# Performance work log

Hardware: AMD Instinct MI355X
Metric: run time of the kernel (lower is better)

## Reference

```python
import jax, jax.numpy as jnp
import numpy as np

LN_EPS = 1e-5


def _ln(x, g, b):
    m = x.mean(-1, keepdims=True)
    v = ((x - m) ** 2).mean(-1, keepdims=True)
    return (x - m) * jax.lax.rsqrt(v + LN_EPS) * g + b


def setup_inputs() -> dict:
    key = jax.random.key(0)
    ks = jax.random.split(key, 8)
    B, S, T, Ds, Dt, H = 2, 1024, 1024, 128, 64, 64

    def w(k, shp):
        return jax.random.normal(k, shp, dtype=jnp.float32) * 0.05

    return {
        "source_features": jax.random.normal(ks[0], (B, S, Ds), dtype=jnp.float32),
        "target_features": jax.random.normal(ks[1], (B, T, Dt), dtype=jnp.float32),
        # source_adapter: Linear(Ds,H) -> LN(H) -> ReLU -> Linear(H,H)
        "sW1": w(ks[2], (Ds, H)), "sb1": jnp.zeros(H), "sg": jnp.ones(H), "sbeta": jnp.zeros(H),
        "sW2": w(ks[3], (H, H)), "sb2": jnp.zeros(H),
        # target_adapter: Linear(Dt,H) -> LN(H) -> ReLU -> Linear(H,H)
        "tW1": w(ks[4], (Dt, H)), "tb1": jnp.zeros(H), "tg": jnp.ones(H), "tbeta": jnp.zeros(H),
        "tW2": w(ks[5], (H, H)), "tb2": jnp.zeros(H),
        # city_features: Linear(2H,H) -> LN(H) -> ReLU
        "cW": w(ks[6], (2 * H, H)), "cb": jnp.zeros(H), "cg": jnp.ones(H), "cbeta": jnp.zeros(H),
        # similarity_module: Linear(H,1) -> Sigmoid
        "simW": w(ks[7], (H, 1)), "simb": jnp.zeros(1),
    }


def reference(source_features, target_features,
              sW1, sb1, sg, sbeta, sW2, sb2,
              tW1, tb1, tg, tbeta, tW2, tb2,
              cW, cb, cg, cbeta, simW, simb):
    H = sW2.shape[1]
    s_ad = jax.nn.relu(_ln(source_features @ sW1 + sb1, sg, sbeta)) @ sW2 + sb2  # [B,S,H]
    t_ad = jax.nn.relu(_ln(target_features @ tW1 + tb1, tg, tbeta)) @ tW2 + tb2  # [B,T,H]

    # concat order in torch is [target, source] on the last dim; split the
    # Linear(2H,H) weight so the [B,T,S,2H] concat is never materialized.
    cW_t, cW_s = cW[:H], cW[H:]
    pre = (t_ad @ cW_t)[:, :, None, :] + (s_ad @ cW_s)[:, None, :, :] + cb  # [B,T,S,H]
    h = jax.nn.relu(_ln(pre, cg, cbeta))
    scores = jax.nn.sigmoid((h @ simW)[..., 0] + simb[0])  # [B,T,S]

    attn = jax.nn.softmax(scores, axis=-1)
    transferred = jnp.einsum('bts,bsh->bth', attn, s_ad)
    gate = jax.nn.sigmoid(t_ad.mean(-1, keepdims=True))
    adapted = t_ad * (1.0 - gate) + transferred * gate  # hidden_dim == target_dim: no proj
    return adapted, scores
```

## Files before the change

### kernel.cpp

```cpp
#include <hip/hip_runtime.h>
#include <math.h>

#define BN 2
#define SN 1024
#define TN 1024
#define DS 128
#define DT 64
#define HN 64
#define LN_EPS 1e-5f

typedef float v2f __attribute__((ext_vector_type(2)));

__device__ __forceinline__ float wave_sum(float v) {
#pragma unroll
  for (int m = 32; m >= 1; m >>= 1) v += __shfl_xor(v, m, 64);
  return v;
}

__device__ __forceinline__ v2f lo2(float4 v) { v2f r = {v.x, v.y}; return r; }
__device__ __forceinline__ v2f hi2(float4 v) { v2f r = {v.z, v.w}; return r; }

__global__ __launch_bounds__(256) void k_adapters(
    const float* __restrict__ src, const float* __restrict__ tgt,
    const float* __restrict__ sW1, const float* __restrict__ sb1,
    const float* __restrict__ sg, const float* __restrict__ sbeta,
    const float* __restrict__ sW2, const float* __restrict__ sb2,
    const float* __restrict__ tW1, const float* __restrict__ tb1,
    const float* __restrict__ tg, const float* __restrict__ tbeta,
    const float* __restrict__ tW2, const float* __restrict__ tb2,
    const float* __restrict__ cW, const float* __restrict__ cb,
    float* __restrict__ s_ad, float* __restrict__ sc, float* __restrict__ sstats,
    float* __restrict__ t_ad, float* __restrict__ tc, float* __restrict__ tstats)
{
  __shared__ float xbuf[4][DS];
  __shared__ float rbuf[4][HN];
  int w = threadIdx.x >> 6, lane = threadIdx.x & 63;

  if (blockIdx.x < 512) {
    int row = blockIdx.x * 4 + w;
    xbuf[w][lane]      = src[row * DS + lane];
    xbuf[w][lane + 64] = src[row * DS + 64 + lane];
    float a0 = 0.f, a1 = 0.f, a2_ = 0.f, a3 = 0.f;
#pragma unroll 8
    for (int k = 0; k < DS; k += 4) {
      a0  = fmaf(xbuf[w][k + 0], sW1[(k + 0) * HN + lane], a0);
      a1  = fmaf(xbuf[w][k + 1], sW1[(k + 1) * HN + lane], a1);
      a2_ = fmaf(xbuf[w][k + 2], sW1[(k + 2) * HN + lane], a2_);
      a3  = fmaf(xbuf[w][k + 3], sW1[(k + 3) * HN + lane], a3);
    }
    float h1 = ((a0 + a1) + (a2_ + a3)) + sb1[lane];
    float s1 = wave_sum(h1), s2 = wave_sum(h1 * h1);
    float m = s1 * (1.f / HN);
    float var = s2 * (1.f / HN) - m * m;
    float r = fmaxf(0.f, (h1 - m) * rsqrtf(var + LN_EPS) * sg[lane] + sbeta[lane]);
    rbuf[w][lane] = r;
    float b0 = 0.f, b1 = 0.f, b2 = 0.f, b3 = 0.f;
#pragma unroll 4
    for (int j = 0; j < HN; j += 4) {
      b0 = fmaf(rbuf[w][j + 0], sW2[(j + 0) * HN + lane], b0);
      b1 = fmaf(rbuf[w][j + 1], sW2[(j + 1) * HN + lane], b1);
      b2 = fmaf(rbuf[w][j + 2], sW2[(j + 2) * HN + lane], b2);
      b3 = fmaf(rbuf[w][j + 3], sW2[(j + 3) * HN + lane], b3);
    }
    float a2 = ((b0 + b1) + (b2 + b3)) + sb2[lane];
    s_ad[row * HN + lane] = a2;
    rbuf[w][lane] = a2;
    float c0 = 0.f, c1 = 0.f, c2 = 0.f, c3 = 0.f;
#pragma unroll 4
    for (int j = 0; j < HN; j += 4) {
      c0 = fmaf(rbuf[w][j + 0], cW[(HN + j + 0) * HN + lane], c0);
      c1 = fmaf(rbuf[w][j + 1], cW[(HN + j + 1) * HN + lane], c1);
      c2 = fmaf(rbuf[w][j + 2], cW[(HN + j + 2) * HN + lane], c2);
      c3 = fmaf(rbuf[w][j + 3], cW[(HN + j + 3) * HN + lane], c3);
    }
    float scv = (c0 + c1) + (c2 + c3);
    sc[row * HN + lane] = scv;
    float bs = wave_sum(scv), qs = wave_sum(scv * scv);
    if (lane == 0) { sstats[row * 2] = bs; sstats[row * 2 + 1] = qs; }
  } else {
    int row = (blockIdx.x - 512) * 4 + w;
    xbuf[w][lane] = tgt[row * DT + lane];
    float a0 = 0.f, a1 = 0.f, a2_ = 0.f, a3 = 0.f;
#pragma unroll 4
    for (int k = 0; k < DT; k += 4) {
      a0  = fmaf(xbuf[w][k + 0], tW1[(k + 0) * HN + lane], a0);
      a1  = fmaf(xbuf[w][k + 1], tW1[(k + 1) * HN + lane], a1);
      a2_ = fmaf(xbuf[w][k + 2], tW1[(k + 2) * HN + lane], a2_);
      a3  = fmaf(xbuf[w][k + 3], tW1[(k + 3) * HN + lane], a3);
    }
    float h1 = ((a0 + a1) + (a2_ + a3)) + tb1[lane];
    float s1 = wave_sum(h1), s2 = wave_sum(h1 * h1);
    float m = s1 * (1.f / HN);
    float var = s2 * (1.f / HN) - m * m;
    float r = fmaxf(0.f, (h1 - m) * rsqrtf(var + LN_EPS) * tg[lane] + tbeta[lane]);
    rbuf[w][lane] = r;
    float b0 = 0.f, b1 = 0.f, b2 = 0.f, b3 = 0.f;
#pragma unroll 4
    for (int j = 0; j < HN; j += 4) {
      b0 = fmaf(rbuf[w][j + 0], tW2[(j + 0) * HN + lane], b0);
      b1 = fmaf(rbuf[w][j + 1], tW2[(j + 1) * HN + lane], b1);
      b2 = fmaf(rbuf[w][j + 2], tW2[(j + 2) * HN + lane], b2);
      b3 = fmaf(rbuf[w][j + 3], tW2[(j + 3) * HN + lane], b3);
    }
    float a2 = ((b0 + b1) + (b2 + b3)) + tb2[lane];
    t_ad[row * HN + lane] = a2;
    float asum = wave_sum(a2);
    float gate = 1.f / (1.f + __expf(-asum * (1.f / HN)));
    rbuf[w][lane] = a2;
    float c0 = 0.f, c1 = 0.f, c2 = 0.f, c3 = 0.f;
#pragma unroll 4
    for (int j = 0; j < HN; j += 4) {
      c0 = fmaf(rbuf[w][j + 0], cW[(j + 0) * HN + lane], c0);
      c1 = fmaf(rbuf[w][j + 1], cW[(j + 1) * HN + lane], c1);
      c2 = fmaf(rbuf[w][j + 2], cW[(j + 2) * HN + lane], c2);
      c3 = fmaf(rbuf[w][j + 3], cW[(j + 3) * HN + lane], c3);
    }
    float tcv = ((c0 + c1) + (c2 + c3)) + cb[lane];
    tc[row * HN + lane] = tcv;
    float A = wave_sum(tcv), Q = wave_sum(tcv * tcv);
    if (lane == 0) { tstats[row * 3] = A; tstats[row * 3 + 1] = Q; tstats[row * 3 + 2] = gate; }
  }
}

#define ROWDW 68
__global__ __launch_bounds__(512) void k_scores(
    const float* __restrict__ cg, const float* __restrict__ cbeta,
    const float* __restrict__ simW, const float* __restrict__ simb,
    const float* __restrict__ sc, const float* __restrict__ sstats,
    const float* __restrict__ tc, const float* __restrict__ tstats,
    float* __restrict__ out_scores)
{
  __shared__ float tile[64 * ROWDW];
  int tid = threadIdx.x;
  int w = tid >> 6, lane = tid & 63;
  int sblk = blockIdx.x & 15;
  int tblk = (blockIdx.x >> 4) & 63;
  int b    = blockIdx.x >> 10;
  int t0 = tblk * 16 + w * 2;
  int rt0 = __builtin_amdgcn_readfirstlane(b * TN + t0);
  int rt1 = rt0 + 1;
  int s0 = sblk * 64;

  float A0  = tstats[rt0 * 3 + 0];
  float Qt0 = tstats[rt0 * 3 + 1];
  float A1  = tstats[rt1 * 3 + 0];
  float Qt1 = tstats[rt1 * 3 + 1];
  const float4* tq0 = (const float4*)(tc + rt0 * HN);
  const float4* tq1 = (const float4*)(tc + rt1 * HN);
  const float4* cgq = (const float4*)cg;
  const float4* cbq = (const float4*)cbeta;
  const float4* swq = (const float4*)simW;
  float simb0 = simb[0];

  const float4* scg = (const float4*)(sc + b * SN * HN);

  {
    int r0s = tid >> 4, gs = tid & 15;
    float4 v0 = scg[(s0 + r0s) * 16 + gs];
    float4 v1 = scg[(s0 + r0s + 32) * 16 + gs];
    *(float4*)&tile[r0s * ROWDW + gs * 4] = v0;
    *(float4*)&tile[(r0s + 32) * ROWDW + gs * 4] = v1;
  }
  __syncthreads();

  const v2f zero2 = {0.f, 0.f};
  const float* tb_ = &tile[lane * ROWDW];
  int s = s0 + lane;
  float2 bq = *(const float2*)&sstats[(b * SN + s) * 2];

  v2f D0a = zero2, D0b = zero2, D1a = zero2, D1b = zero2;
#pragma unroll
  for (int g = 0; g < 16; ++g) {
    float4 v = *(const float4*)&tb_[g * 4];
    float4 ta = tq0[g]; float4 tbv = tq1[g];
    D0a = __builtin_elementwise_fma(lo2(ta),  lo2(v), D0a);
    D0b = __builtin_elementwise_fma(hi2(ta),  hi2(v), D0b);
    D1a = __builtin_elementwise_fma(lo2(tbv), lo2(v), D1a);
    D1b = __builtin_elementwise_fma(hi2(tbv), hi2(v), D1b);
  }
  v2f Ds0 = D0a + D0b, Ds1 = D1a + D1b;
  float D_0 = Ds0.x + Ds0.y;
  float D_1 = Ds1.x + Ds1.y;

  float mean0  = (A0 + bq.x) * (1.f / HN);
  float var0   = (Qt0 + bq.y + 2.f * D_0) * (1.f / HN) - mean0 * mean0;
  float alpha0 = rsqrtf(var0 + LN_EPS);
  float mean1  = (A1 + bq.x) * (1.f / HN);
  float var1   = (Qt1 + bq.y + 2.f * D_1) * (1.f / HN) - mean1 * mean1;
  float alpha1 = rsqrtf(var1 + LN_EPS);

  v2f m0 = {mean0, mean0}, a0v = {alpha0, alpha0};
  v2f m1 = {mean1, mean1}, a1v = {alpha1, alpha1};
  v2f dt0a = zero2, dt0b = zero2, dt1a = zero2, dt1b = zero2;

#pragma unroll
  for (int g = 0; g < 16; ++g) {
    float4 v  = *(const float4*)&tb_[g * 4];
    float4 c4 = cgq[g]; float4 b4 = cbq[g]; float4 w4 = swq[g];
    float4 ta = tq0[g]; float4 tbv = tq1[g];
    { v2f u = lo2(v) + lo2(ta);  v2f z = u - m0; v2f P = a0v * lo2(c4);
      v2f n = __builtin_elementwise_fma(z, P, lo2(b4));
      v2f r = __builtin_elementwise_max(n, zero2);
      dt0a = __builtin_elementwise_fma(r, lo2(w4), dt0a); }
    { v2f u = hi2(v) + hi2(ta);  v2f z = u - m0; v2f P = a0v * hi2(c4);
      v2f n = __builtin_elementwise_fma(z, P, hi2(b4));
      v2f r = __builtin_elementwise_max(n, zero2);
      dt0b = __builtin_elementwise_fma(r, hi2(w4), dt0b); }
    { v2f u = lo2(v) + lo2(tbv); v2f z = u - m1; v2f P = a1v * lo2(c4);
      v2f n = __builtin_elementwise_fma(z, P, lo2(b4));
      v2f r = __builtin_elementwise_max(n, zero2);
      dt1a = __builtin_elementwise_fma(r, lo2(w4), dt1a); }
    { v2f u = hi2(v) + hi2(tbv); v2f z = u - m1; v2f P = a1v * hi2(c4);
      v2f n = __builtin_elementwise_fma(z, P, hi2(b4));
      v2f r = __builtin_elementwise_max(n, zero2);
      dt1b = __builtin_elementwise_fma(r, hi2(w4), dt1b); }
  }
  v2f dd0 = dt0a + dt0b, dd1 = dt1a + dt1b;
  float dot0 = dd0.x + dd0.y;
  float dot1 = dd1.x + dd1.y;
  float score0 = 1.f / (1.f + __expf(-(dot0 + simb0)));
  float score1 = 1.f / (1.f + __expf(-(dot1 + simb0)));
  out_scores[rt0 * SN + s] = score0;
  out_scores[rt1 * SN + s] = score1;
}

__global__ __launch_bounds__(256, 4) void k_xfer(
    const float* __restrict__ scores, const float* __restrict__ s_ad,
    float* __restrict__ xpart, float* __restrict__ epart)
{
  __shared__ float eLDS[4][16][64];
  __shared__ float part[4][16][64];
  __shared__ float esum[4][16];
  int tid = threadIdx.x;
  int w = __builtin_amdgcn_readfirstlane(tid >> 6);
  int lane = tid & 63;
  int sblk = blockIdx.x & 3;
  int tblk = (blockIdx.x >> 2) & 63;
  int b    = blockIdx.x >> 8;
  int t0 = tblk * 16;
  int soff = sblk * 256 + w * 64;

#pragma unroll 4
  for (int t = 0; t < 16; ++t) {
    int rt = __builtin_amdgcn_readfirstlane(b * TN + t0 + t);
    float ev = __expf(scores[rt * SN + soff + lane]);
    eLDS[w][t][lane] = ev;
    float es = wave_sum(ev);
    if (lane == 0) esum[w][t] = es;
  }

  const float* sadb = s_ad + b * SN * HN;
  float acc[16];
#pragma unroll
  for (int t = 0; t < 16; ++t) acc[t] = 0.f;
#pragma unroll 4
  for (int si4 = 0; si4 < 16; ++si4) {
    int sbase = soff + si4 * 4;
    float sv0 = sadb[(sbase + 0) * HN + lane];
    float sv1 = sadb[(sbase + 1) * HN + lane];
    float sv2 = sadb[(sbase + 2) * HN + lane];
    float sv3 = sadb[(sbase + 3) * HN + lane];
#pragma unroll
    for (int t = 0; t < 16; ++t) {
      float4 e4 = *(const float4*)&eLDS[w][t][si4 * 4];
      acc[t] = fmaf(e4.x, sv0, acc[t]);
      acc[t] = fmaf(e4.y, sv1, acc[t]);
      acc[t] = fmaf(e4.z, sv2, acc[t]);
      acc[t] = fmaf(e4.w, sv3, acc[t]);
    }
  }

#pragma unroll
  for (int t = 0; t < 16; ++t) part[w][t][lane] = acc[t];
  __syncthreads();
#pragma unroll
  for (int k = 0; k < 4; ++k) {
    int c2 = tid + k * 256;
    int t = c2 >> 6, h = c2 & 63;
    float sum = part[0][t][h] + part[1][t][h] + part[2][t][h] + part[3][t][h];
    int rt = b * TN + t0 + t;
    xpart[(rt * 4 + sblk) * HN + h] = sum;
  }
  if (tid < 16) {
    float es = esum[0][tid] + esum[1][tid] + esum[2][tid] + esum[3][tid];
    int rt = b * TN + t0 + tid;
    epart[rt * 4 + sblk] = es;
  }
}

__global__ __launch_bounds__(256) void k_final(
    const float* __restrict__ xpart, const float* __restrict__ epart,
    const float* __restrict__ t_ad, const float* __restrict__ tstats,
    float* __restrict__ out_adapted)
{
  int tid = threadIdx.x;
  int tl = tid >> 6, h = tid & 63;
  int rt = blockIdx.x * 4 + tl;
  float x = xpart[(rt * 4 + 0) * HN + h] + xpart[(rt * 4 + 1) * HN + h]
          + xpart[(rt * 4 + 2) * HN + h] + xpart[(rt * 4 + 3) * HN + h];
  float es = epart[rt * 4 + 0] + epart[rt * 4 + 1]
           + epart[rt * 4 + 2] + epart[rt * 4 + 3];
  float tr = x / es;
  float gate = tstats[rt * 3 + 2];
  float tad = t_ad[rt * HN + h];
  out_adapted[rt * HN + h] = tad * (1.f - gate) + tr * gate;
}

extern "C" void kernel_launch(void* const* d_in, const int* in_sizes, int n_in,
                              void* d_out, int out_size, void* d_ws, size_t ws_size,
                              hipStream_t stream) {
  const float* src   = (const float*)d_in[0];
  const float* tgt   = (const float*)d_in[1];
  const float* sW1   = (const float*)d_in[2];
  const float* sb1   = (const float*)d_in[3];
  const float* sg    = (const float*)d_in[4];
  const float* sbeta = (const float*)d_in[5];
  const float* sW2   = (const float*)d_in[6];
  const float* sb2   = (const float*)d_in[7];
  const float* tW1   = (const float*)d_in[8];
  const float* tb1   = (const float*)d_in[9];
  const float* tg    = (const float*)d_in[10];
  const float* tbeta = (const float*)d_in[11];
  const float* tW2   = (const float*)d_in[12];
  const float* tb2   = (const float*)d_in[13];
  const float* cW    = (const float*)d_in[14];
  const float* cb    = (const float*)d_in[15];
  const float* cg    = (const float*)d_in[16];
  const float* cbeta = (const float*)d_in[17];
  const float* simW  = (const float*)d_in[18];
  const float* simb  = (const float*)d_in[19];

  float* ws     = (float*)d_ws;
  float* s_ad   = ws;
  float* sc     = ws + 131072;
  float* sstats = ws + 262144;
  float* t_ad   = ws + 266240;
  float* tc     = ws + 397312;
  float* tstats = ws + 528384;
  float* xpart  = ws + 534528;
  float* epart  = ws + 1058816;

  float* out_adapted = (float*)d_out;
  float* out_scores  = (float*)d_out + 131072;

  hipLaunchKernelGGL(k_adapters, dim3(1024), dim3(256), 0, stream,
                     src, tgt, sW1, sb1, sg, sbeta, sW2, sb2,
                     tW1, tb1, tg, tbeta, tW2, tb2, cW, cb,
                     s_ad, sc, sstats, t_ad, tc, tstats);
  hipLaunchKernelGGL(k_scores, dim3(BN * 64 * 16), dim3(512), 0, stream,
                     cg, cbeta, simW, simb, sc, sstats, tc, tstats, out_scores);
  hipLaunchKernelGGL(k_xfer, dim3(BN * 64 * 4), dim3(256), 0, stream,
                     out_scores, s_ad, xpart, epart);
  hipLaunchKernelGGL(k_final, dim3(512), dim3(256), 0, stream,
                     xpart, epart, t_ad, tstats, out_adapted);
}
```

Baseline: 154.3 us.

## Fuse softmax-transfer and final gating into one kernel using readlane broadcasts

Merges the transfer and final kernels into a single kernel in which each block handles 4 target rows across the full source range, with each wave covering a quarter of the sources. Exp scores are broadcast through readlane instead of being staged in LDS. This removes the xpart/epart workspace round trip and one kernel launch. In exchange each block reuses each s_ad load for only 4 target rows instead of 16, which raises L2 traffic for s_ad, and the per-iteration readlanes add scalar work.

```diff
diff --git a/kernel.cpp b/kernel.cpp
--- a/kernel.cpp
+++ b/kernel.cpp
@@ -19,6 +19,10 @@
 
 __device__ __forceinline__ v2f lo2(float4 v) { v2f r = {v.x, v.y}; return r; }
 __device__ __forceinline__ v2f hi2(float4 v) { v2f r = {v.z, v.w}; return r; }
+
+__device__ __forceinline__ float rl(float v, int l) {
+  return __int_as_float(__builtin_amdgcn_readlane(__float_as_int(v), l));
+}
 
 __global__ __launch_bounds__(256) void k_adapters(
     const float* __restrict__ src, const float* __restrict__ tgt,
@@ -224,82 +228,59 @@
   out_scores[rt1 * SN + s] = score1;
 }
 
-__global__ __launch_bounds__(256, 4) void k_xfer(
+__global__ __launch_bounds__(256) void k_transfer(
     const float* __restrict__ scores, const float* __restrict__ s_ad,
-    float* __restrict__ xpart, float* __restrict__ epart)
-{
-  __shared__ float eLDS[4][16][64];
-  __shared__ float part[4][16][64];
-  __shared__ float esum[4][16];
-  int tid = threadIdx.x;
-  int w = __builtin_amdgcn_readfirstlane(tid >> 6);
-  int lane = tid & 63;
-  int sblk = blockIdx.x & 3;
-  int tblk = (blockIdx.x >> 2) & 63;
-  int b    = blockIdx.x >> 8;
-  int t0 = tblk * 16;
-  int soff = sblk * 256 + w * 64;
-
-#pragma unroll 4
-  for (int t = 0; t < 16; ++t) {
-    int rt = __builtin_amdgcn_readfirstlane(b * TN + t0 + t);
-    float ev = __expf(scores[rt * SN + soff + lane]);
-    eLDS[w][t][lane] = ev;
-    float es = wave_sum(ev);
-    if (lane == 0) esum[w][t] = es;
-  }
-
-  const float* sadb = s_ad + b * SN * HN;
-  float acc[16];
-#pragma unroll
-  for (int t = 0; t < 16; ++t) acc[t] = 0.f;
-#pragma unroll 4
-  for (int si4 = 0; si4 < 16; ++si4) {
-    int sbase = soff + si4 * 4;
-    float sv0 = sadb[(sbase + 0) * HN + lane];
-    float sv1 = sadb[(sbase + 1) * HN + lane];
-    float sv2 = sadb[(sbase + 2) * HN + lane];
-    float sv3 = sadb[(sbase + 3) * HN + lane];
-#pragma unroll
-    for (int t = 0; t < 16; ++t) {
-      float4 e4 = *(const float4*)&eLDS[w][t][si4 * 4];
-      acc[t] = fmaf(e4.x, sv0, acc[t]);
-      acc[t] = fmaf(e4.y, sv1, acc[t]);
-      acc[t] = fmaf(e4.z, sv2, acc[t]);
-      acc[t] = fmaf(e4.w, sv3, acc[t]);
-    }
-  }
-
-#pragma unroll
-  for (int t = 0; t < 16; ++t) part[w][t][lane] = acc[t];
-  __syncthreads();
-#pragma unroll
-  for (int k = 0; k < 4; ++k) {
-    int c2 = tid + k * 256;
-    int t = c2 >> 6, h = c2 & 63;
-    float sum = part[0][t][h] + part[1][t][h] + part[2][t][h] + part[3][t][h];
-    int rt = b * TN + t0 + t;
-    xpart[(rt * 4 + sblk) * HN + h] = sum;
-  }
-  if (tid < 16) {
-    float es = esum[0][tid] + esum[1][tid] + esum[2][tid] + esum[3][tid];
-    int rt = b * TN + t0 + tid;
-    epart[rt * 4 + sblk] = es;
-  }
-}
-
-__global__ __launch_bounds__(256) void k_final(
-    const float* __restrict__ xpart, const float* __restrict__ epart,
     const float* __restrict__ t_ad, const float* __restrict__ tstats,
     float* __restrict__ out_adapted)
 {
+  __shared__ float part[4][4][64];
+  __shared__ float esumLDS[4][4];
   int tid = threadIdx.x;
-  int tl = tid >> 6, h = tid & 63;
-  int rt = blockIdx.x * 4 + tl;
-  float x = xpart[(rt * 4 + 0) * HN + h] + xpart[(rt * 4 + 1) * HN + h]
-          + xpart[(rt * 4 + 2) * HN + h] + xpart[(rt * 4 + 3) * HN + h];
-  float es = epart[rt * 4 + 0] + epart[rt * 4 + 1]
-           + epart[rt * 4 + 2] + epart[rt * 4 + 3];
+  int w = tid >> 6, lane = tid & 63;
+  int tblk = blockIdx.x & 255;
+  int b    = blockIdx.x >> 8;
+  int rtb  = b * TN + tblk * 4;
+  const float* sadb = s_ad + b * SN * HN;
+
+  float acc0 = 0.f, acc1 = 0.f, acc2 = 0.f, acc3 = 0.f;
+  float es0 = 0.f, es1 = 0.f, es2 = 0.f, es3 = 0.f;
+  int s0w = w * 256;
+
+#pragma unroll
+  for (int sub = 0; sub < 4; ++sub) {
+    int sbase = s0w + sub * 64;
+    float e0 = __expf(scores[(rtb + 0) * SN + sbase + lane]);
+    float e1 = __expf(scores[(rtb + 1) * SN + sbase + lane]);
+    float e2 = __expf(scores[(rtb + 2) * SN + sbase + lane]);
+    float e3 = __expf(scores[(rtb + 3) * SN + sbase + lane]);
+    es0 += e0; es1 += e1; es2 += e2; es3 += e3;
+    const float* srow = sadb + sbase * HN + lane;
+#pragma unroll 16
+    for (int si = 0; si < 64; ++si) {
+      float sv = srow[si * HN];
+      acc0 = fmaf(rl(e0, si), sv, acc0);
+      acc1 = fmaf(rl(e1, si), sv, acc1);
+      acc2 = fmaf(rl(e2, si), sv, acc2);
+      acc3 = fmaf(rl(e3, si), sv, acc3);
+    }
+  }
+
+  part[w][0][lane] = acc0;
+  part[w][1][lane] = acc1;
+  part[w][2][lane] = acc2;
+  part[w][3][lane] = acc3;
+  float t0s = wave_sum(es0), t1s = wave_sum(es1);
+  float t2s = wave_sum(es2), t3s = wave_sum(es3);
+  if (lane == 0) {
+    esumLDS[w][0] = t0s; esumLDS[w][1] = t1s;
+    esumLDS[w][2] = t2s; esumLDS[w][3] = t3s;
+  }
+  __syncthreads();
+
+  int t = w, h = lane;
+  float x  = part[0][t][h] + part[1][t][h] + part[2][t][h] + part[3][t][h];
+  float es = esumLDS[0][t] + esumLDS[1][t] + esumLDS[2][t] + esumLDS[3][t];
+  int rt = rtb + t;
   float tr = x / es;
   float gate = tstats[rt * 3 + 2];
   float tad = t_ad[rt * HN + h];
@@ -337,8 +318,6 @@
   float* t_ad   = ws + 266240;
   float* tc     = ws + 397312;
   float* tstats = ws + 528384;
-  float* xpart  = ws + 534528;
-  float* epart  = ws + 1058816;
 
   float* out_adapted = (float*)d_out;
   float* out_scores  = (float*)d_out + 131072;
@@ -349,8 +328,6 @@
                      s_ad, sc, sstats, t_ad, tc, tstats);
   hipLaunchKernelGGL(k_scores, dim3(BN * 64 * 16), dim3(512), 0, stream,
                      cg, cbeta, simW, simb, sc, sstats, tc, tstats, out_scores);
-  hipLaunchKernelGGL(k_xfer, dim3(BN * 64 * 4), dim3(256), 0, stream,
-                     out_scores, s_ad, xpart, epart);
-  hipLaunchKernelGGL(k_final, dim3(512), dim3(256), 0, stream,
-                     xpart, epart, t_ad, tstats, out_adapted);
-}
+  hipLaunchKernelGGL(k_transfer, dim3(BN * 256), dim3(256), 0, stream,
+                     out_scores, s_ad, t_ad, tstats, out_adapted);
+}
```

Measured after the change: 146.6 us (median of 2 runs). 5.0% less time.
